# Performance work log

Hardware: AMD Instinct MI355X
Metric: run time of the kernel (lower is better)

The kernel has to match this reference:

```python
import jax, jax.numpy as jnp
import numpy as np
import math

B, N, D_MODEL, H, D_HEAD = 2, 2048, 1024, 16, 64
EPS = 1e-6

def setup_inputs() -> dict:
    key = jax.random.key(0)
    ks = jax.random.split(key, 6)
    s = 1.0 / math.sqrt(D_MODEL)
    return {
        "X": jax.random.normal(ks[0], (B, N, D_MODEL), dtype=jnp.float32),
        "Wq": jax.random.normal(ks[1], (D_MODEL, H * D_HEAD), dtype=jnp.float32) * s,
        "Wk": jax.random.normal(ks[2], (D_MODEL, H * D_HEAD), dtype=jnp.float32) * s,
        "Wv": jax.random.normal(ks[3], (D_MODEL, H * D_HEAD), dtype=jnp.float32) * s,
        "Wo": jax.random.normal(ks[4], (H * D_HEAD, D_MODEL), dtype=jnp.float32) * s,
        "bo": jnp.zeros((D_MODEL,), dtype=jnp.float32),
    }

def reference(X, Wq, Wk, Wv, Wo, bo):
    b, n, _ = X.shape
    # project and split heads -> [b, h, n, d_head]
    def heads(Y):
        return Y.reshape(b, n, H, D_HEAD).transpose(0, 2, 1, 3)
    Q = heads(X @ Wq)
    K = heads(X @ Wk)
    V = heads(X @ Wv)
    # per-head L2 normalization of Q and K
    Q = Q / (jnp.linalg.norm(Q, axis=-1, keepdims=True) + EPS)
    K = K / (jnp.linalg.norm(K, axis=-1, keepdims=True) + EPS)
    # scores [b, h, n, n]
    A = jnp.einsum("bhqd,bhkd->bhqk", Q, K) / math.sqrt(D_HEAD)
    causal = jnp.triu(jnp.ones((n, n), dtype=bool), k=1)
    A = jnp.where(causal, -jnp.inf, A)
    A = jax.nn.softmax(A, axis=-1)
    V_hat = jnp.einsum("bhqk,bhkd->bhqd", A, V)
    V_hat = V_hat.transpose(0, 2, 1, 3).reshape(b, n, H * D_HEAD)
    return V_hat @ Wo + bo
```

## Files before the change

kernel.cpp:

```cpp
#include <hip/hip_runtime.h>
#include <hip/hip_bf16.h>
#include <math.h>

#define BATCH 2
#define NSEQ  2048
#define DM    1024
#define NH    16
#define DH    64
#define EPS_N 1e-6f

typedef unsigned short u16;
typedef __attribute__((ext_vector_type(8))) short short8;
typedef __attribute__((ext_vector_type(8))) unsigned short u16x8;
typedef __attribute__((ext_vector_type(4))) unsigned short u16x4;
typedef __attribute__((ext_vector_type(4))) float f32x4;

__device__ __forceinline__ u16 f2bf(float x) {
  __hip_bfloat16 h = __float2bfloat16(x);
  return *reinterpret_cast<u16*>(&h);
}

__device__ __forceinline__ void gl_lds16(const u16* g, u16* lds_base) {
  __builtin_amdgcn_global_load_lds(
      (__attribute__((address_space(1))) void*)g,
      (__attribute__((address_space(3))) void*)lds_base, 16, 0, 0);
}

__global__ __launch_bounds__(256) void prep(
    const float* __restrict__ X,
    const float* __restrict__ w0, const float* __restrict__ w1,
    const float* __restrict__ w2, const float* __restrict__ w3,
    u16* __restrict__ Xb, u16* __restrict__ WT) {
  const int id = blockIdx.x, tid = threadIdx.x;
  if (id >= 1024) {
    size_t base = ((size_t)(id - 1024) * 256 + tid) * 8;
    float4 f0 = *(const float4*)&X[base];
    float4 f1 = *(const float4*)&X[base + 4];
    u16x8 v;
    v[0] = f2bf(f0.x); v[1] = f2bf(f0.y); v[2] = f2bf(f0.z); v[3] = f2bf(f0.w);
    v[4] = f2bf(f1.x); v[5] = f2bf(f1.y); v[6] = f2bf(f1.z); v[7] = f2bf(f1.w);
    *(u16x8*)&Xb[base] = v;
    return;
  }
  const int z = id >> 8, xy = id & 255, bx = xy & 15, by = xy >> 4;
  const float* in = (z == 0) ? w0 : (z == 1) ? w1 : (z == 2) ? w2 : w3;
  u16* o = WT + (size_t)z * DM * DM;
  __shared__ u16 T[64][65];
  const int n0 = bx * 64, k0 = by * 64;
  #pragma unroll
  for (int i = 0; i < 4; i++) {
    int c = tid + 256 * i, row = c >> 4, col4 = c & 15;
    float4 f = *(const float4*)&in[(size_t)(k0 + row) * DM + n0 + col4 * 4];
    T[row][col4 * 4 + 0] = f2bf(f.x);
    T[row][col4 * 4 + 1] = f2bf(f.y);
    T[row][col4 * 4 + 2] = f2bf(f.z);
    T[row][col4 * 4 + 3] = f2bf(f.w);
  }
  __syncthreads();
  #pragma unroll
  for (int i = 0; i < 2; i++) {
    int c = tid + 256 * i, row = c >> 3, col8 = c & 7;
    u16x8 v;
    #pragma unroll
    for (int e = 0; e < 8; e++) v[e] = T[col8 * 8 + e][row];
    *(u16x8*)&o[(size_t)(n0 + row) * DM + k0 + col8 * 8] = v;
  }
}

#define GEMM64x128_MAINLOOP(Aptr, Btptr)                                       \
  __shared__ u16 As[64 * 64];                                                  \
  __shared__ u16 Bs[128 * 64];                                                 \
  const int tid = threadIdx.x, w = tid >> 6, lane = tid & 63;                  \
  const int ml = lane & 15, quad = lane >> 4;                                  \
  const int m0 = blockIdx.y * 64, n0 = blockIdx.x * 128;                       \
  const int wm = w & 1, wn = w >> 1;                                           \
  const int srow = lane >> 3;                      \
  const int scol = ((lane & 7) ^ srow) * 8;         \
  f32x4 acc[2][4];                                                             \
  _Pragma("unroll") for (int mi = 0; mi < 2; mi++)                             \
    _Pragma("unroll") for (int ni = 0; ni < 4; ni++)                           \
      _Pragma("unroll") for (int e = 0; e < 4; e++) acc[mi][ni][e] = 0.f;      \
  for (int k0 = 0; k0 < DM; k0 += 64) {                                        \
    __syncthreads();                                                           \
    _Pragma("unroll") for (int L = 0; L < 2; L++) {                            \
      int I = w * 2 + L;                                    \
      gl_lds16(Aptr + (size_t)(m0 + I * 8 + srow) * DM + k0 + scol,            \
               As + I * 512);                                                  \
    }                                                                          \
    _Pragma("unroll") for (int L = 0; L < 4; L++) {                            \
      int I = w * 4 + L;                                   \
      gl_lds16(Btptr + (size_t)(n0 + I * 8 + srow) * DM + k0 + scol,           \
               Bs + I * 512);                                                  \
    }                                                                          \
    __syncthreads();                                                           \
    _Pragma("unroll") for (int kk = 0; kk < 64; kk += 32) {                    \
      const int kc = kk >> 3;                          \
      short8 am[2], bn[4];                                                     \
      _Pragma("unroll") for (int i = 0; i < 2; i++) {                          \
        int ra = wm * 32 + i * 16 + ml;                                        \
        am[i] = *(const short8*)&As[ra * 64 + (((quad + kc) ^ (ra & 7)) * 8)]; \
      }                                                                        \
      _Pragma("unroll") for (int i = 0; i < 4; i++) {                          \
        int rb = wn * 64 + i * 16 + ml;                                        \
        bn[i] = *(const short8*)&Bs[rb * 64 + (((quad + kc) ^ (rb & 7)) * 8)]; \
      }                                                                        \
      _Pragma("unroll") for (int mi = 0; mi < 2; mi++)                         \
        _Pragma("unroll") for (int ni = 0; ni < 4; ni++)                       \
          acc[mi][ni] = __builtin_amdgcn_mfma_f32_16x16x32_bf16(               \
              am[mi], bn[ni], acc[mi][ni], 0, 0, 0);                           \
    }                                                                          \
  }

__global__ __launch_bounds__(256) void gemm_qkv128(
    const u16* __restrict__ Xb, const u16* __restrict__ WT,
    u16* __restrict__ Qo, u16* __restrict__ Ko, u16* __restrict__ Vt) {
  const u16* Bt = WT + (size_t)blockIdx.z * DM * DM;
  GEMM64x128_MAINLOOP(Xb, Bt)
  const int z = blockIdx.z;
  if (z < 2) {
    u16* OutQK = (z == 0) ? Qo : Ko;
    const float qsc = (z == 0) ? 0.125f : 1.0f;
    const int h = (n0 >> 6) + wn;
    #pragma unroll
    for (int mi = 0; mi < 2; mi++) {
      int mrow0 = m0 + wm * 32 + mi * 16 + quad * 4;
      int b = mrow0 >> 11, tok0 = mrow0 & (NSEQ - 1);
      #pragma unroll
      for (int r = 0; r < 4; r++) {
        float ss = 0.f;
        #pragma unroll
        for (int ni = 0; ni < 4; ni++) ss += acc[mi][ni][r] * acc[mi][ni][r];
        ss += __shfl_xor(ss, 1, 64);
        ss += __shfl_xor(ss, 2, 64);
        ss += __shfl_xor(ss, 4, 64);
        ss += __shfl_xor(ss, 8, 64);
        float sc = qsc / (sqrtf(ss) + EPS_N);
        #pragma unroll
        for (int ni = 0; ni < 4; ni++)
          OutQK[((size_t)(b * NH + h) * NSEQ + tok0 + r) * DH + ni * 16 + ml] =
              f2bf(acc[mi][ni][r] * sc);
      }
    }
  } else {
    #pragma unroll
    for (int mi = 0; mi < 2; mi++) {
      int mrow0 = m0 + wm * 32 + mi * 16 + quad * 4;
      int b = mrow0 >> 11, tok0 = mrow0 & (NSEQ - 1);
      #pragma unroll
      for (int ni = 0; ni < 4; ni++) {
        int n = n0 + wn * 64 + ni * 16 + ml;
        int h = n >> 6, d = n & 63;
        u16x4 pk;
        #pragma unroll
        for (int r = 0; r < 4; r++) pk[r] = f2bf(acc[mi][ni][r]);
        *(u16x4*)&Vt[((size_t)(b * NH + h) * DH + d) * NSEQ + tok0] = pk;
      }
    }
  }
}

__global__ __launch_bounds__(256) void gemm_proj128(
    const u16* __restrict__ A, const u16* __restrict__ BtW,
    const float* __restrict__ bias, float* __restrict__ out) {
  GEMM64x128_MAINLOOP(A, BtW)
  #pragma unroll
  for (int ni = 0; ni < 4; ni++) {
    int n = n0 + wn * 64 + ni * 16 + ml;
    float bz = bias[n];
    #pragma unroll
    for (int mi = 0; mi < 2; mi++) {
      int mrow0 = m0 + wm * 32 + mi * 16 + quad * 4;
      #pragma unroll
      for (int r = 0; r < 4; r++)
        out[(size_t)(mrow0 + r) * DM + n] = acc[mi][ni][r] + bz;
    }
  }
}

__global__ __launch_bounds__(512) void flash_attn(
    const u16* __restrict__ Qb, const u16* __restrict__ Kb,
    const u16* __restrict__ Vt, u16* __restrict__ vhat) {
  const int tid = threadIdx.x, w = tid >> 6, lane = tid & 63;
  const int ml = lane & 15, quad = lane >> 4;
  const int wq = w & 3, wk = w >> 2;
  const int bh = blockIdx.x;
  const int bb = bh >> 4, hb = bh & 15;
  const int pairY = blockIdx.y;
  const u16* Qh = Qb + (size_t)bh * NSEQ * DH;
  const u16* Kh = Kb + (size_t)bh * NSEQ * DH;
  const u16* Vth = Vt + (size_t)bh * DH * NSEQ;

  __shared__ u16 Ks [64 * 64];
  __shared__ u16 VsT[64 * 64];
  __shared__ u16 Ps [8][16][40];
  __shared__ float Os[4][16][66];
  __shared__ float Ls[4][16];

  const int srow8 = lane >> 3;
  const int sch   = lane & 7;
  const int sslot = sch ^ srow8;

  for (int ph = 0; ph < 2; ph++) {
    const int qb64 = ph ? (31 - pairY) : pairY;
    const int q0 = qb64 * 64;
    const int ntiles = qb64 + 1;

    short8 aq[2];
    #pragma unroll
    for (int c = 0; c < 2; c++)
      aq[c] = *(const short8*)&Qh[(size_t)(q0 + wq * 16 + ml) * DH + c * 32 + quad * 8];

    f32x4 oacc[4];
    #pragma unroll
    for (int n = 0; n < 4; n++)
      #pragma unroll
      for (int e = 0; e < 4; e++) oacc[n][e] = 0.f;
    float l_[4] = {0.f, 0.f, 0.f, 0.f};

    u16x8 kreg, vreg;
    kreg = *(const u16x8*)&Kh[(size_t)(w * 8 + srow8) * DH + sch * 8];
    vreg = *(const u16x8*)&Vth[(size_t)(w * 8 + srow8) * NSEQ + sch * 8];

    for (int t = 0; t < ntiles; t++) {
      const int j0 = t * 64;
      __syncthreads();
      *(u16x8*)&Ks [(w * 8 + srow8) * 64 + sslot * 8] = kreg;
      *(u16x8*)&VsT[(w * 8 + srow8) * 64 + sslot * 8] = vreg;
      __syncthreads();

      if (t + 1 < ntiles) {
        const int j1 = j0 + 64;
        kreg = *(const u16x8*)&Kh[(size_t)(j1 + w * 8 + srow8) * DH + sch * 8];
        vreg = *(const u16x8*)&Vth[(size_t)(w * 8 + srow8) * NSEQ + j1 + sch * 8];
      }

      f32x4 sacc[2];
      #pragma unroll
      for (int n = 0; n < 2; n++)
        #pragma unroll
        for (int e = 0; e < 4; e++) sacc[n][e] = 0.f;
      #pragma unroll
      for (int c = 0; c < 2; c++)
        #pragma unroll
        for (int n = 0; n < 2; n++) {
          int kr = wk * 32 + n * 16 + ml;
          short8 bf = *(const short8*)&Ks[kr * 64 + (((c * 4 + quad) ^ (kr & 7)) * 8)];
          sacc[n] = __builtin_amdgcn_mfma_f32_16x16x32_bf16(aq[c], bf, sacc[n], 0, 0, 0);
        }

      const bool lastt = (t == ntiles - 1);
      float p[2][4];
      #pragma unroll
      for (int n = 0; n < 2; n++) {
        int j = j0 + wk * 32 + n * 16 + ml;
        #pragma unroll
        for (int r = 0; r < 4; r++) {
          int q = q0 + wq * 16 + quad * 4 + r;
          float e = __expf(sacc[n][r]);
          p[n][r] = (lastt && j > q) ? 0.f : e;
          l_[r] += p[n][r];
        }
      }

      #pragma unroll
      for (int n = 0; n < 2; n++)
        #pragma unroll
        for (int r = 0; r < 4; r++)
          Ps[w][quad * 4 + r][n * 16 + ml] = f2bf(p[n][r]);

      short8 ap = *(const short8*)&Ps[w][ml][quad * 8];
      #pragma unroll
      for (int n = 0; n < 4; n++) {
        int dr = n * 16 + ml;
        short8 bv = *(const short8*)&VsT[dr * 64 + (((wk * 4 + quad) ^ (dr & 7)) * 8)];
        oacc[n] = __builtin_amdgcn_mfma_f32_16x16x32_bf16(ap, bv, oacc[n], 0, 0, 0);
      }
    }

    float lred[4];
    #pragma unroll
    for (int r = 0; r < 4; r++) {
      float lv = l_[r];
      lv += __shfl_xor(lv, 1, 64);
      lv += __shfl_xor(lv, 2, 64);
      lv += __shfl_xor(lv, 4, 64);
      lv += __shfl_xor(lv, 8, 64);
      lred[r] = lv;
    }
    if (wk == 0) {
      #pragma unroll
      for (int n = 0; n < 4; n++)
        #pragma unroll
        for (int r = 0; r < 4; r++)
          Os[wq][quad * 4 + r][n * 16 + ml] = oacc[n][r];
      if (ml == 0) {
        #pragma unroll
        for (int r = 0; r < 4; r++) Ls[wq][quad * 4 + r] = lred[r];
      }
    }
    __syncthreads();
    if (wk == 1) {
      #pragma unroll
      for (int r = 0; r < 4; r++) {
        float inv = 1.f / (lred[r] + Ls[wq][quad * 4 + r]);
        int q = q0 + wq * 16 + quad * 4 + r;
        #pragma unroll
        for (int n = 0; n < 4; n++) {
          float o = oacc[n][r] + Os[wq][quad * 4 + r][n * 16 + ml];
          vhat[((size_t)(bb * NSEQ + q)) * DM + hb * DH + n * 16 + ml] =
              f2bf(o * inv);
        }
      }
    }
    __syncthreads();
  }
}

extern "C" void kernel_launch(void* const* d_in, const int* in_sizes, int n_in,
                              void* d_out, int out_size, void* d_ws, size_t ws_size,
                              hipStream_t stream) {
  const float* X  = (const float*)d_in[0];
  const float* Wq = (const float*)d_in[1];
  const float* Wk = (const float*)d_in[2];
  const float* Wv = (const float*)d_in[3];
  const float* Wo = (const float*)d_in[4];
  const float* bo = (const float*)d_in[5];
  float* out = (float*)d_out;

  const size_t NE = (size_t)BATCH * NSEQ * DM;
  u16* Qb   = (u16*)d_ws;
  u16* Kb   = Qb + NE;
  u16* Vt   = Kb + NE;
  u16* XbVh = Vt + NE;
  u16* WT   = XbVh + NE;

  prep        <<<dim3(3072),      256, 0, stream>>>(X, Wq, Wk, Wv, Wo, XbVh, WT);
  gemm_qkv128 <<<dim3(8, 64, 3),  256, 0, stream>>>(XbVh, WT, Qb, Kb, Vt);
  flash_attn  <<<dim3(32, 16),    512, 0, stream>>>(Qb, Kb, Vt, XbVh);
  gemm_proj128<<<dim3(8, 64, 1),  256, 0, stream>>>(XbVh, WT + 3 * (size_t)DM * DM,
                                                    bo, out);
}
```

Measured before the change: 182.2 us.

## Fuse X bf16 conversion into QKV GEMM with double-buffered LDS pipeline

Drops the separate X fp32-to-bf16 pass in prep. The QKV GEMM now loads fp32 X straight into registers, converts it and writes it swizzled into LDS. The main loop is double-buffered so the next tile's X load and async B-to-LDS stage overlap the current MFMA compute, with one barrier per iteration. The grid is also reordered so M varies fastest. The cost is that X is read as fp32 three times, once per z slice, instead of bf16, and LDS use doubles.

```diff
diff --git a/kernel.cpp b/kernel.cpp
--- a/kernel.cpp
+++ b/kernel.cpp
@@ -27,21 +27,10 @@
 }
 
 __global__ __launch_bounds__(256) void prep(
-    const float* __restrict__ X,
     const float* __restrict__ w0, const float* __restrict__ w1,
     const float* __restrict__ w2, const float* __restrict__ w3,
-    u16* __restrict__ Xb, u16* __restrict__ WT) {
+    u16* __restrict__ WT) {
   const int id = blockIdx.x, tid = threadIdx.x;
-  if (id >= 1024) {
-    size_t base = ((size_t)(id - 1024) * 256 + tid) * 8;
-    float4 f0 = *(const float4*)&X[base];
-    float4 f1 = *(const float4*)&X[base + 4];
-    u16x8 v;
-    v[0] = f2bf(f0.x); v[1] = f2bf(f0.y); v[2] = f2bf(f0.z); v[3] = f2bf(f0.w);
-    v[4] = f2bf(f1.x); v[5] = f2bf(f1.y); v[6] = f2bf(f1.z); v[7] = f2bf(f1.w);
-    *(u16x8*)&Xb[base] = v;
-    return;
-  }
   const int z = id >> 8, xy = id & 255, bx = xy & 15, by = xy >> 4;
   const float* in = (z == 0) ? w0 : (z == 1) ? w1 : (z == 2) ? w2 : w3;
   u16* o = WT + (size_t)z * DM * DM;
@@ -67,55 +56,98 @@
   }
 }
 
-#define GEMM64x128_MAINLOOP(Aptr, Btptr)                                       \
-  __shared__ u16 As[64 * 64];                                                  \
-  __shared__ u16 Bs[128 * 64];                                                 \
-  const int tid = threadIdx.x, w = tid >> 6, lane = tid & 63;                  \
-  const int ml = lane & 15, quad = lane >> 4;                                  \
-  const int m0 = blockIdx.y * 64, n0 = blockIdx.x * 128;                       \
-  const int wm = w & 1, wn = w >> 1;                                           \
-  const int srow = lane >> 3;                      \
-  const int scol = ((lane & 7) ^ srow) * 8;         \
-  f32x4 acc[2][4];                                                             \
-  _Pragma("unroll") for (int mi = 0; mi < 2; mi++)                             \
-    _Pragma("unroll") for (int ni = 0; ni < 4; ni++)                           \
-      _Pragma("unroll") for (int e = 0; e < 4; e++) acc[mi][ni][e] = 0.f;      \
-  for (int k0 = 0; k0 < DM; k0 += 64) {                                        \
-    __syncthreads();                                                           \
-    _Pragma("unroll") for (int L = 0; L < 2; L++) {                            \
-      int I = w * 2 + L;                                    \
-      gl_lds16(Aptr + (size_t)(m0 + I * 8 + srow) * DM + k0 + scol,            \
-               As + I * 512);                                                  \
-    }                                                                          \
-    _Pragma("unroll") for (int L = 0; L < 4; L++) {                            \
-      int I = w * 4 + L;                                   \
-      gl_lds16(Btptr + (size_t)(n0 + I * 8 + srow) * DM + k0 + scol,           \
-               Bs + I * 512);                                                  \
-    }                                                                          \
-    __syncthreads();                                                           \
+#define GEMM_COMPUTE(Asrc, Bsrc)                                               \
+  do {                                                                         \
     _Pragma("unroll") for (int kk = 0; kk < 64; kk += 32) {                    \
       const int kc = kk >> 3;                          \
       short8 am[2], bn[4];                                                     \
       _Pragma("unroll") for (int i = 0; i < 2; i++) {                          \
         int ra = wm * 32 + i * 16 + ml;                                        \
-        am[i] = *(const short8*)&As[ra * 64 + (((quad + kc) ^ (ra & 7)) * 8)]; \
+        am[i] = *(const short8*)&(Asrc)[ra * 64 +                              \
+                                        (((quad + kc) ^ (ra & 7)) * 8)];       \
       }                                                                        \
       _Pragma("unroll") for (int i = 0; i < 4; i++) {                          \
         int rb = wn * 64 + i * 16 + ml;                                        \
-        bn[i] = *(const short8*)&Bs[rb * 64 + (((quad + kc) ^ (rb & 7)) * 8)]; \
+        bn[i] = *(const short8*)&(Bsrc)[rb * 64 +                              \
+                                        (((quad + kc) ^ (rb & 7)) * 8)];       \
       }                                                                        \
       _Pragma("unroll") for (int mi = 0; mi < 2; mi++)                         \
         _Pragma("unroll") for (int ni = 0; ni < 4; ni++)                       \
           acc[mi][ni] = __builtin_amdgcn_mfma_f32_16x16x32_bf16(               \
               am[mi], bn[ni], acc[mi][ni], 0, 0, 0);                           \
     }                                                                          \
-  }
+  } while (0)
 
 __global__ __launch_bounds__(256) void gemm_qkv128(
-    const u16* __restrict__ Xb, const u16* __restrict__ WT,
+    const float* __restrict__ X, const u16* __restrict__ WT,
     u16* __restrict__ Qo, u16* __restrict__ Ko, u16* __restrict__ Vt) {
   const u16* Bt = WT + (size_t)blockIdx.z * DM * DM;
-  GEMM64x128_MAINLOOP(Xb, Bt)
+  __shared__ u16 As[2][64 * 64];
+  __shared__ u16 Bs[2][128 * 64];
+  const int tid = threadIdx.x, w = tid >> 6, lane = tid & 63;
+  const int ml = lane & 15, quad = lane >> 4;
+  const int m0 = blockIdx.x * 64, n0 = blockIdx.y * 128;
+  const int wm = w & 1, wn = w >> 1;
+  const int srow = lane >> 3;
+  const int scol = ((lane & 7) ^ srow) * 8;
+  const int arow = tid >> 2, ac4 = tid & 3;
+  const int aslot0 = (ac4 * 2) ^ (arow & 7);
+  const int aslot1 = (ac4 * 2 + 1) ^ (arow & 7);
+  f32x4 acc[2][4];
+  #pragma unroll
+  for (int mi = 0; mi < 2; mi++)
+    #pragma unroll
+    for (int ni = 0; ni < 4; ni++)
+      #pragma unroll
+      for (int e = 0; e < 4; e++) acc[mi][ni][e] = 0.f;
+
+  float4 af[4];
+#define QKV_A_LOAD(koff)                                                       \
+  do {                                                                         \
+    _Pragma("unroll") for (int i = 0; i < 4; i++)                              \
+      af[i] = *(const float4*)&X[(size_t)(m0 + arow) * DM + (koff) +           \
+                                 ac4 * 16 + i * 4];                            \
+  } while (0)
+#define QKV_B_STAGE(koff, buf)                                                 \
+  do {                                                                         \
+    _Pragma("unroll") for (int L = 0; L < 4; L++) {                            \
+      int I = w * 4 + L;                                                       \
+      gl_lds16(Bt + (size_t)(n0 + I * 8 + srow) * DM + (koff) + scol,          \
+               Bs[buf] + I * 512);                                             \
+    }                                                                          \
+  } while (0)
+#define QKV_A_WRITE(buf)                                                       \
+  do {                                                                         \
+    u16x8 aw0, aw1;                                                            \
+    aw0[0] = f2bf(af[0].x); aw0[1] = f2bf(af[0].y);                            \
+    aw0[2] = f2bf(af[0].z); aw0[3] = f2bf(af[0].w);                            \
+    aw0[4] = f2bf(af[1].x); aw0[5] = f2bf(af[1].y);                            \
+    aw0[6] = f2bf(af[1].z); aw0[7] = f2bf(af[1].w);                            \
+    aw1[0] = f2bf(af[2].x); aw1[1] = f2bf(af[2].y);                            \
+    aw1[2] = f2bf(af[2].z); aw1[3] = f2bf(af[2].w);                            \
+    aw1[4] = f2bf(af[3].x); aw1[5] = f2bf(af[3].y);                            \
+    aw1[6] = f2bf(af[3].z); aw1[7] = f2bf(af[3].w);                            \
+    *(u16x8*)&As[buf][arow * 64 + aslot0 * 8] = aw0;                           \
+    *(u16x8*)&As[buf][arow * 64 + aslot1 * 8] = aw1;                           \
+  } while (0)
+
+  QKV_A_LOAD(0);
+  QKV_B_STAGE(0, 0);
+  QKV_A_WRITE(0);
+  __syncthreads();
+  int cur = 0;
+  for (int k0 = 0; k0 < DM; k0 += 64) {
+    const bool nxt = (k0 + 64 < DM);
+    if (nxt) {
+      QKV_A_LOAD(k0 + 64);
+      QKV_B_STAGE(k0 + 64, cur ^ 1);
+    }
+    GEMM_COMPUTE(As[cur], Bs[cur]);
+    if (nxt) QKV_A_WRITE(cur ^ 1);
+    __syncthreads();
+    cur ^= 1;
+  }
+
   const int z = blockIdx.z;
   if (z < 2) {
     u16* OutQK = (z == 0) ? Qo : Ko;
@@ -162,7 +194,36 @@
 __global__ __launch_bounds__(256) void gemm_proj128(
     const u16* __restrict__ A, const u16* __restrict__ BtW,
     const float* __restrict__ bias, float* __restrict__ out) {
-  GEMM64x128_MAINLOOP(A, BtW)
+  __shared__ u16 As[64 * 64];
+  __shared__ u16 Bs[128 * 64];
+  const int tid = threadIdx.x, w = tid >> 6, lane = tid & 63;
+  const int ml = lane & 15, quad = lane >> 4;
+  const int m0 = blockIdx.y * 64, n0 = blockIdx.x * 128;
+  const int wm = w & 1, wn = w >> 1;
+  const int srow = lane >> 3;
+  const int scol = ((lane & 7) ^ srow) * 8;
+  f32x4 acc[2][4];
+  #pragma unroll
+  for (int mi = 0; mi < 2; mi++)
+    #pragma unroll
+    for (int ni = 0; ni < 4; ni++)
+      #pragma unroll
+      for (int e = 0; e < 4; e++) acc[mi][ni][e] = 0.f;
+  for (int k0 = 0; k0 < DM; k0 += 64) {
+    __syncthreads();
+    #pragma unroll
+    for (int L = 0; L < 2; L++) {
+      int I = w * 2 + L;
+      gl_lds16(A + (size_t)(m0 + I * 8 + srow) * DM + k0 + scol, As + I * 512);
+    }
+    #pragma unroll
+    for (int L = 0; L < 4; L++) {
+      int I = w * 4 + L;
+      gl_lds16(BtW + (size_t)(n0 + I * 8 + srow) * DM + k0 + scol, Bs + I * 512);
+    }
+    __syncthreads();
+    GEMM_COMPUTE(As, Bs);
+  }
   #pragma unroll
   for (int ni = 0; ni < 4; ni++) {
     int n = n0 + wn * 64 + ni * 16 + ml;
@@ -331,12 +392,12 @@
   u16* Qb   = (u16*)d_ws;
   u16* Kb   = Qb + NE;
   u16* Vt   = Kb + NE;
-  u16* XbVh = Vt + NE;
-  u16* WT   = XbVh + NE;
-
-  prep        <<<dim3(3072),      256, 0, stream>>>(X, Wq, Wk, Wv, Wo, XbVh, WT);
-  gemm_qkv128 <<<dim3(8, 64, 3),  256, 0, stream>>>(XbVh, WT, Qb, Kb, Vt);
-  flash_attn  <<<dim3(32, 16),    512, 0, stream>>>(Qb, Kb, Vt, XbVh);
-  gemm_proj128<<<dim3(8, 64, 1),  256, 0, stream>>>(XbVh, WT + 3 * (size_t)DM * DM,
+  u16* vhat = Vt + NE;
+  u16* WT   = vhat + NE;
+
+  prep        <<<dim3(1024),      256, 0, stream>>>(Wq, Wk, Wv, Wo, WT);
+  gemm_qkv128 <<<dim3(64, 8, 3),  256, 0, stream>>>(X, WT, Qb, Kb, Vt);
+  flash_attn  <<<dim3(32, 16),    512, 0, stream>>>(Qb, Kb, Vt, vhat);
+  gemm_proj128<<<dim3(8, 64, 1),  256, 0, stream>>>(vhat, WT + 3 * (size_t)DM * DM,
                                                     bo, out);
 }
```

Result: no change. 185.6 us (+1.9%).

## Double-buffer QKV GEMM LDS tiles and shrink projection GEMM tile to 64x64

Applied to the files above, without the earlier changes.

The QKV projection GEMM now keeps two LDS buffers and issues the next k-tile's global-to-LDS loads before computing the current one. This is meant to overlap memory latency with MFMA work and drops one barrier per iteration. The output projection GEMM uses 64x64 tiles with twice as many blocks, aiming to fill more CUs at the cost of less reuse per block. Double buffering doubles LDS use, which may lower occupancy.

```diff
diff --git a/kernel.cpp b/kernel.cpp
--- a/kernel.cpp
+++ b/kernel.cpp
@@ -67,55 +67,80 @@
   }
 }
 
-#define GEMM64x128_MAINLOOP(Aptr, Btptr)                                       \
-  __shared__ u16 As[64 * 64];                                                  \
-  __shared__ u16 Bs[128 * 64];                                                 \
+#define GEMM_STAGE_A(Aptr, koff, Adst, NSLAB_W)                                \
+  do {                                                                         \
+    _Pragma("unroll") for (int L = 0; L < (NSLAB_W); L++) {                    \
+      int I = w * (NSLAB_W) + L;                                               \
+      gl_lds16(Aptr + (size_t)(m0 + I * 8 + srow) * DM + (koff) + scol,        \
+               (Adst) + I * 512);                                              \
+    }                                                                          \
+  } while (0)
+#define GEMM_STAGE_B(Btptr, koff, Bdst, NSLAB_W)                               \
+  do {                                                                         \
+    _Pragma("unroll") for (int L = 0; L < (NSLAB_W); L++) {                    \
+      int I = w * (NSLAB_W) + L;                                               \
+      gl_lds16(Btptr + (size_t)(n0 + I * 8 + srow) * DM + (koff) + scol,       \
+               (Bdst) + I * 512);                                              \
+    }                                                                          \
+  } while (0)
+
+#define GEMM_COMMON_DECLS                                                      \
   const int tid = threadIdx.x, w = tid >> 6, lane = tid & 63;                  \
   const int ml = lane & 15, quad = lane >> 4;                                  \
-  const int m0 = blockIdx.y * 64, n0 = blockIdx.x * 128;                       \
   const int wm = w & 1, wn = w >> 1;                                           \
   const int srow = lane >> 3;                      \
-  const int scol = ((lane & 7) ^ srow) * 8;         \
-  f32x4 acc[2][4];                                                             \
-  _Pragma("unroll") for (int mi = 0; mi < 2; mi++)                             \
-    _Pragma("unroll") for (int ni = 0; ni < 4; ni++)                           \
-      _Pragma("unroll") for (int e = 0; e < 4; e++) acc[mi][ni][e] = 0.f;      \
-  for (int k0 = 0; k0 < DM; k0 += 64) {                                        \
-    __syncthreads();                                                           \
-    _Pragma("unroll") for (int L = 0; L < 2; L++) {                            \
-      int I = w * 2 + L;                                    \
-      gl_lds16(Aptr + (size_t)(m0 + I * 8 + srow) * DM + k0 + scol,            \
-               As + I * 512);                                                  \
-    }                                                                          \
-    _Pragma("unroll") for (int L = 0; L < 4; L++) {                            \
-      int I = w * 4 + L;                                   \
-      gl_lds16(Btptr + (size_t)(n0 + I * 8 + srow) * DM + k0 + scol,           \
-               Bs + I * 512);                                                  \
-    }                                                                          \
-    __syncthreads();                                                           \
-    _Pragma("unroll") for (int kk = 0; kk < 64; kk += 32) {                    \
-      const int kc = kk >> 3;                          \
-      short8 am[2], bn[4];                                                     \
-      _Pragma("unroll") for (int i = 0; i < 2; i++) {                          \
-        int ra = wm * 32 + i * 16 + ml;                                        \
-        am[i] = *(const short8*)&As[ra * 64 + (((quad + kc) ^ (ra & 7)) * 8)]; \
-      }                                                                        \
-      _Pragma("unroll") for (int i = 0; i < 4; i++) {                          \
-        int rb = wn * 64 + i * 16 + ml;                                        \
-        bn[i] = *(const short8*)&Bs[rb * 64 + (((quad + kc) ^ (rb & 7)) * 8)]; \
-      }                                                                        \
-      _Pragma("unroll") for (int mi = 0; mi < 2; mi++)                         \
-        _Pragma("unroll") for (int ni = 0; ni < 4; ni++)                       \
-          acc[mi][ni] = __builtin_amdgcn_mfma_f32_16x16x32_bf16(               \
-              am[mi], bn[ni], acc[mi][ni], 0, 0, 0);                           \
-    }                                                                          \
-  }
+  const int scol = ((lane & 7) ^ srow) * 8;
 
 __global__ __launch_bounds__(256) void gemm_qkv128(
     const u16* __restrict__ Xb, const u16* __restrict__ WT,
     u16* __restrict__ Qo, u16* __restrict__ Ko, u16* __restrict__ Vt) {
   const u16* Bt = WT + (size_t)blockIdx.z * DM * DM;
-  GEMM64x128_MAINLOOP(Xb, Bt)
+  __shared__ u16 As[2][64 * 64];
+  __shared__ u16 Bs[2][128 * 64];
+  GEMM_COMMON_DECLS
+  const int m0 = blockIdx.y * 64, n0 = blockIdx.x * 128;
+  f32x4 acc[2][4];
+  #pragma unroll
+  for (int mi = 0; mi < 2; mi++)
+    #pragma unroll
+    for (int ni = 0; ni < 4; ni++)
+      #pragma unroll
+      for (int e = 0; e < 4; e++) acc[mi][ni][e] = 0.f;
+
+  GEMM_STAGE_A(Xb, 0, As[0], 2);
+  GEMM_STAGE_B(Bt, 0, Bs[0], 4);
+  __syncthreads();
+  int cur = 0;
+  for (int k0 = 0; k0 < DM; k0 += 64) {
+    if (k0 + 64 < DM) {
+      GEMM_STAGE_A(Xb, k0 + 64, As[cur ^ 1], 2);
+      GEMM_STAGE_B(Bt, k0 + 64, Bs[cur ^ 1], 4);
+    }
+    #pragma unroll
+    for (int kk = 0; kk < 64; kk += 32) {
+      const int kc = kk >> 3;
+      short8 am[2], bn[4];
+      #pragma unroll
+      for (int i = 0; i < 2; i++) {
+        int ra = wm * 32 + i * 16 + ml;
+        am[i] = *(const short8*)&As[cur][ra * 64 + (((quad + kc) ^ (ra & 7)) * 8)];
+      }
+      #pragma unroll
+      for (int i = 0; i < 4; i++) {
+        int rb = wn * 64 + i * 16 + ml;
+        bn[i] = *(const short8*)&Bs[cur][rb * 64 + (((quad + kc) ^ (rb & 7)) * 8)];
+      }
+      #pragma unroll
+      for (int mi = 0; mi < 2; mi++)
+        #pragma unroll
+        for (int ni = 0; ni < 4; ni++)
+          acc[mi][ni] = __builtin_amdgcn_mfma_f32_16x16x32_bf16(
+              am[mi], bn[ni], acc[mi][ni], 0, 0, 0);
+    }
+    __syncthreads();
+    cur ^= 1;
+  }
+
   const int z = blockIdx.z;
   if (z < 2) {
     u16* OutQK = (z == 0) ? Qo : Ko;
@@ -162,10 +187,47 @@
 __global__ __launch_bounds__(256) void gemm_proj128(
     const u16* __restrict__ A, const u16* __restrict__ BtW,
     const float* __restrict__ bias, float* __restrict__ out) {
-  GEMM64x128_MAINLOOP(A, BtW)
+  __shared__ u16 As[64 * 64];
+  __shared__ u16 Bs[64 * 64];
+  GEMM_COMMON_DECLS
+  const int m0 = blockIdx.y * 64, n0 = blockIdx.x * 64;
+  f32x4 acc[2][2];
   #pragma unroll
-  for (int ni = 0; ni < 4; ni++) {
-    int n = n0 + wn * 64 + ni * 16 + ml;
+  for (int mi = 0; mi < 2; mi++)
+    #pragma unroll
+    for (int ni = 0; ni < 2; ni++)
+      #pragma unroll
+      for (int e = 0; e < 4; e++) acc[mi][ni][e] = 0.f;
+  for (int k0 = 0; k0 < DM; k0 += 64) {
+    __syncthreads();
+    GEMM_STAGE_A(A, k0, As, 2);
+    GEMM_STAGE_B(BtW, k0, Bs, 2);
+    __syncthreads();
+    #pragma unroll
+    for (int kk = 0; kk < 64; kk += 32) {
+      const int kc = kk >> 3;
+      short8 am[2], bn[2];
+      #pragma unroll
+      for (int i = 0; i < 2; i++) {
+        int ra = wm * 32 + i * 16 + ml;
+        am[i] = *(const short8*)&As[ra * 64 + (((quad + kc) ^ (ra & 7)) * 8)];
+      }
+      #pragma unroll
+      for (int i = 0; i < 2; i++) {
+        int rb = wn * 32 + i * 16 + ml;
+        bn[i] = *(const short8*)&Bs[rb * 64 + (((quad + kc) ^ (rb & 7)) * 8)];
+      }
+      #pragma unroll
+      for (int mi = 0; mi < 2; mi++)
+        #pragma unroll
+        for (int ni = 0; ni < 2; ni++)
+          acc[mi][ni] = __builtin_amdgcn_mfma_f32_16x16x32_bf16(
+              am[mi], bn[ni], acc[mi][ni], 0, 0, 0);
+    }
+  }
+  #pragma unroll
+  for (int ni = 0; ni < 2; ni++) {
+    int n = n0 + wn * 32 + ni * 16 + ml;
     float bz = bias[n];
     #pragma unroll
     for (int mi = 0; mi < 2; mi++) {
@@ -337,6 +399,6 @@
   prep        <<<dim3(3072),      256, 0, stream>>>(X, Wq, Wk, Wv, Wo, XbVh, WT);
   gemm_qkv128 <<<dim3(8, 64, 3),  256, 0, stream>>>(XbVh, WT, Qb, Kb, Vt);
   flash_attn  <<<dim3(32, 16),    512, 0, stream>>>(Qb, Kb, Vt, XbVh);
-  gemm_proj128<<<dim3(8, 64, 1),  256, 0, stream>>>(XbVh, WT + 3 * (size_t)DM * DM,
+  gemm_proj128<<<dim3(16, 64),    256, 0, stream>>>(XbVh, WT + 3 * (size_t)DM * DM,
                                                     bo, out);
 }
```

Result: no change. 180.4 us (median of 5 runs) (-1.0%).
